# Performance work log

Measured on AMD Instinct MI355X. Metric: run time of the kernel, lower is better.

The kernel has to match this reference:

```python
import jax, jax.numpy as jnp
import numpy as np

N_NODES = 50000
N_EDGES = 600000
IN_DIM = 128
LATENT = 128
OUT_DIM = 40
NUM_LAYERS = 2


def setup_inputs() -> dict:
    key = jax.random.key(0)
    ks = jax.random.split(key, 8)
    nodes_feats = jax.random.normal(ks[0], (N_NODES, IN_DIM), dtype=jnp.float32)
    adj_list = jax.random.randint(ks[1], (N_EDGES, 2), 0, N_NODES, dtype=jnp.int64)
    s_in = 1.0 / np.sqrt(IN_DIM)
    s_cb = 1.0 / np.sqrt(2 * LATENT)
    s_out = 1.0 / np.sqrt(LATENT)
    W_in = jax.random.uniform(ks[2], (IN_DIM, LATENT), jnp.float32, -s_in, s_in)
    b_in = jnp.zeros((LATENT,), jnp.float32)
    W_comb = jax.random.uniform(ks[3], (NUM_LAYERS, 2 * LATENT, LATENT), jnp.float32, -s_cb, s_cb)
    b_comb = jnp.zeros((NUM_LAYERS, LATENT), jnp.float32)
    W_out = jax.random.uniform(ks[4], (LATENT, OUT_DIM), jnp.float32, -s_out, s_out)
    b_out = jnp.zeros((OUT_DIM,), jnp.float32)
    return {"nodes_feats": nodes_feats, "adj_list": adj_list, "W_in": W_in, "b_in": b_in,
            "W_comb": W_comb, "b_comb": b_comb, "W_out": W_out, "b_out": b_out}


def reference(nodes_feats, adj_list, W_in, b_in, W_comb, b_comb, W_out, b_out):
    n = nodes_feats.shape[0]
    fro = adj_list[:, 0]
    to = adj_list[:, 1]
    # initialize: project input features to latent space
    h = jax.nn.relu(nodes_feats @ W_in + b_in)  # [N, LATENT]
    # in-degree for mean aggregation (replaces per-node Python stack+mean)
    deg = jax.ops.segment_sum(jnp.ones(fro.shape[0], h.dtype), to, num_segments=n)
    inv_deg = 1.0 / jnp.maximum(deg, 1.0)  # guard isolated nodes
    for l in range(W_comb.shape[0]):
        # gather neighbor feats along edges, scatter-add to destinations, mean
        msg = jax.ops.segment_sum(h[fro], to, num_segments=n) * inv_deg[:, None]
        # combine: ReLU(Linear([node || message]))
        h = jax.nn.relu(jnp.concatenate([h, msg], axis=-1) @ W_comb[l] + b_comb[l])
    # output head (logits for CrossEntropyLoss)
    return h @ W_out + b_out
```

## Files before the change

kernel.cpp:

```cpp
#include <hip/hip_runtime.h>
#include <hip/hip_fp16.h>

#define N_NODES 50000
#define N_EDGES 600000
#define NBLK 49

typedef unsigned int u32;
typedef _Float16 v8h __attribute__((ext_vector_type(8)));
typedef _Float16 v4h __attribute__((ext_vector_type(4)));
typedef float v4f __attribute__((ext_vector_type(4)));

__device__ __forceinline__ float2 h2f2(u32 u) {
    __half2 h = *(__half2*)&u;
    return __half22float2(h);
}

__global__ void k_detect(const int* __restrict__ adj_w, int* __restrict__ mode) {
    if (threadIdx.x == 0 && blockIdx.x == 0) {
        int allz = 1;
        for (int i = 1; i < 128; i += 2)
            if (adj_w[i] != 0) { allz = 0; break; }
        *mode = allz;
    }
}
__device__ __forceinline__ int adj_to(const int* a, int m, int e) {
    return m ? a[4 * e + 2] : a[2 * e + 1];
}
__device__ __forceinline__ int adj_fro(const int* a, int m, int e) {
    return m ? a[4 * e] : a[2 * e];
}

__global__ void k_count(const int* __restrict__ adj_w, const int* __restrict__ mode,
                        int* __restrict__ deg) {
    int e = blockIdx.x * blockDim.x + threadIdx.x;
    if (e < N_EDGES) atomicAdd(&deg[adj_to(adj_w, *mode, e)], 1);
}

__global__ void k_scan1(const int* __restrict__ deg, int* __restrict__ row_ptr,
                        int* __restrict__ bsum) {
    __shared__ int s[1024];
    int tid = threadIdx.x, i = blockIdx.x * 1024 + tid;
    int v = (i < N_NODES) ? deg[i] : 0;
    s[tid] = v;
    __syncthreads();
    for (int off = 1; off < 1024; off <<= 1) {
        int t = (tid >= off) ? s[tid - off] : 0;
        __syncthreads();
        s[tid] += t;
        __syncthreads();
    }
    if (i < N_NODES) row_ptr[i] = s[tid] - v;
    if (tid == 1023) bsum[blockIdx.x] = s[1023];
}

__global__ void k_scan2(int* __restrict__ bsum) {
    __shared__ int s[64];
    int tid = threadIdx.x;
    int v = (tid < NBLK) ? bsum[tid] : 0;
    s[tid] = v;
    __syncthreads();
    for (int off = 1; off < 64; off <<= 1) {
        int t = (tid >= off) ? s[tid - off] : 0;
        __syncthreads();
        s[tid] += t;
        __syncthreads();
    }
    if (tid < NBLK) bsum[tid] = s[tid] - v;
}

__global__ void k_scan3(const int* __restrict__ deg, int* __restrict__ row_ptr,
                        const int* __restrict__ bsum, int* __restrict__ cursor,
                        float* __restrict__ inv_deg) {
    int i = blockIdx.x * 1024 + threadIdx.x;
    if (i < N_NODES) {
        int rp = row_ptr[i] + bsum[i >> 10];
        row_ptr[i] = rp;
        cursor[i] = rp;
        inv_deg[i] = 1.0f / fmaxf((float)deg[i], 1.0f);
    }
    if (i == 0) row_ptr[N_NODES] = N_EDGES;
}

__global__ void k_fill(const int* __restrict__ adj_w, const int* __restrict__ mode,
                       int* __restrict__ cursor, int* __restrict__ edge_src) {
    int e = blockIdx.x * blockDim.x + threadIdx.x;
    if (e < N_EDGES) {
        int m = *mode;
        int to = adj_to(adj_w, m, e);
        int slot = atomicAdd(&cursor[to], 1);
        edge_src[slot] = adj_fro(adj_w, m, e);
    }
}

__global__ void k_wprep(const float* __restrict__ W_in,
                        const float* __restrict__ W_comb,
                        const float* __restrict__ W_out,
                        _Float16* __restrict__ WinT,
                        _Float16* __restrict__ WcombT,
                        _Float16* __restrict__ WoutT) {
    int idx = blockIdx.x * blockDim.x + threadIdx.x;
    if (idx < 16384) {
        int n = idx & 127, k = idx >> 7;
        WinT[n * 128 + k] = (_Float16)W_in[k * 128 + n];
    } else if (idx < 16384 + 65536) {
        int j = idx - 16384;
        int l = j >> 15, r = j & 32767;
        int n = r & 127, k = r >> 7;
        WcombT[l * 32768 + n * 256 + k] = (_Float16)W_comb[l * 32768 + k * 128 + n];
    } else if (idx < 16384 + 65536 + 6144) {
        int j = idx - 81920;
        int n = j >> 7, k = j & 127;
        WoutT[n * 128 + k] = (n < 40) ? (_Float16)W_out[k * 40 + n] : (_Float16)0.f;
    }
}

__global__ __launch_bounds__(256) void k_gather(const u32* __restrict__ h2,
                                                u32* __restrict__ msg2,
                                                const int* __restrict__ row_ptr,
                                                const int* __restrict__ edge_src,
                                                const float* __restrict__ inv_deg) {
    const int w = threadIdx.x >> 6, l = threadIdx.x & 63;
    const int wid = blockIdx.x * 4 + w, nw = gridDim.x * 4;
    for (int row = wid; row < N_NODES; row += nw) {
        const int e0 = row_ptr[row], e1 = row_ptr[row + 1];
        float ax = 0.f, ay = 0.f;
        for (int bse = e0; bse < e1; bse += 8) {
            u32 v[8];
#pragma unroll
            for (int i = 0; i < 8; i++) {
                int ee = bse + i;
                int idx = (ee < e1) ? ee : (e1 - 1);
                v[i] = h2[(size_t)edge_src[idx] * 64 + l];
            }
#pragma unroll
            for (int i = 0; i < 8; i++) {
                if (bse + i < e1) {
                    float2 f = h2f2(v[i]);
                    ax += f.x;
                    ay += f.y;
                }
            }
        }
        const float inv = inv_deg[row];
        __half2 o = __floats2half2_rn(ax * inv, ay * inv);
        msg2[(size_t)row * 64 + l] = *(u32*)&o;
    }
}

__global__ __launch_bounds__(256, 2) void k_in(const float* __restrict__ X,
                                               const _Float16* __restrict__ WT,
                                               const float* __restrict__ bias,
                                               _Float16* __restrict__ h) {
    __shared__ __align__(16) _Float16 xs[32][136];
    const int t0 = threadIdx.x, w = t0 >> 6, l = t0 & 63;
    const int R0 = blockIdx.x * 32;
    const float4* X4 = (const float4*)X;
#pragma unroll
    for (int i = 0; i < 4; i++) {
        int idx = i * 256 + t0;
        int row = idx >> 5, c4 = idx & 31;
        int rr = R0 + row;
        if (rr > N_NODES - 1) rr = N_NODES - 1;
        float4 v = X4[(size_t)rr * 32 + c4];
        v4h hv = {(_Float16)v.x, (_Float16)v.y, (_Float16)v.z, (_Float16)v.w};
        *(v4h*)&xs[row][c4 * 4] = hv;
    }
    const int ch = w & 1, rh = w >> 1;
    v8h wf[4][4];
#pragma unroll
    for (int t = 0; t < 4; t++)
#pragma unroll
        for (int s = 0; s < 4; s++) {
            int n = ch * 64 + t * 16 + (l & 15);
            int k = s * 32 + (l >> 4) * 8;
            wf[t][s] = *(const v8h*)&WT[n * 128 + k];
        }
    v4f acc[4];
#pragma unroll
    for (int t = 0; t < 4; t++) acc[t] = (v4f){0.f, 0.f, 0.f, 0.f};
    __syncthreads();
#pragma unroll
    for (int s = 0; s < 4; s++) {
        v8h a = *(const v8h*)&xs[rh * 16 + (l & 15)][s * 32 + (l >> 4) * 8];
#pragma unroll
        for (int t = 0; t < 4; t++)
            acc[t] = __builtin_amdgcn_mfma_f32_16x16x32_f16(a, wf[t][s], acc[t], 0, 0, 0);
    }
#pragma unroll
    for (int t = 0; t < 4; t++) {
        int col = ch * 64 + t * 16 + (l & 15);
        float b = bias[col];
#pragma unroll
        for (int i = 0; i < 4; i++) {
            int row = R0 + rh * 16 + (l >> 4) * 4 + i;
            if (row < N_NODES)
                h[(size_t)row * 128 + col] = (_Float16)fmaxf(acc[t][i] + b, 0.f);
        }
    }
}

__global__ __launch_bounds__(256, 2) void k_layer(const _Float16* __restrict__ hin,
                                                  const _Float16* __restrict__ msg,
                                                  const _Float16* __restrict__ WT,
                                                  const float* __restrict__ bias,
                                                  _Float16* __restrict__ hout) {
    __shared__ __align__(16) _Float16 xs[64][264];
    const int t0 = threadIdx.x, w = t0 >> 6, l = t0 & 63;
    const int R0 = blockIdx.x * 64;
    const uint4* h4 = (const uint4*)hin;
    const uint4* m4 = (const uint4*)msg;
#pragma unroll
    for (int i = 0; i < 8; i++) {
        int idx = i * 256 + t0;
        int row = idx >> 5, c16 = idx & 31;
        int rr = R0 + row;
        if (rr > N_NODES - 1) rr = N_NODES - 1;
        uint4 v = (c16 < 16) ? h4[(size_t)rr * 16 + c16] : m4[(size_t)rr * 16 + (c16 - 16)];
        *(uint4*)&xs[row][c16 * 8] = v;
    }
    const int ch = w & 1, rh = w >> 1;
    v8h wf[4][8];
#pragma unroll
    for (int t = 0; t < 4; t++)
#pragma unroll
        for (int s = 0; s < 8; s++) {
            int n = ch * 64 + t * 16 + (l & 15);
            int k = s * 32 + (l >> 4) * 8;
            wf[t][s] = *(const v8h*)&WT[n * 256 + k];
        }
    v4f acc[2][4];
#pragma unroll
    for (int sub = 0; sub < 2; sub++)
#pragma unroll
        for (int t = 0; t < 4; t++) acc[sub][t] = (v4f){0.f, 0.f, 0.f, 0.f};
    __syncthreads();
#pragma unroll
    for (int s = 0; s < 8; s++) {
#pragma unroll
        for (int sub = 0; sub < 2; sub++) {
            v8h a = *(const v8h*)&xs[rh * 32 + sub * 16 + (l & 15)][s * 32 + (l >> 4) * 8];
#pragma unroll
            for (int t = 0; t < 4; t++)
                acc[sub][t] = __builtin_amdgcn_mfma_f32_16x16x32_f16(a, wf[t][s], acc[sub][t], 0, 0, 0);
        }
    }
#pragma unroll
    for (int sub = 0; sub < 2; sub++)
#pragma unroll
        for (int t = 0; t < 4; t++) {
            int col = ch * 64 + t * 16 + (l & 15);
            float b = bias[col];
#pragma unroll
            for (int i = 0; i < 4; i++) {
                int row = R0 + rh * 32 + sub * 16 + (l >> 4) * 4 + i;
                if (row < N_NODES)
                    hout[(size_t)row * 128 + col] = (_Float16)fmaxf(acc[sub][t][i] + b, 0.f);
            }
        }
}

__global__ __launch_bounds__(256, 2) void k_out(const _Float16* __restrict__ hin,
                                                const _Float16* __restrict__ WT,
                                                const float* __restrict__ bias,
                                                float* __restrict__ outp) {
    __shared__ __align__(16) _Float16 xs[64][136];
    const int t0 = threadIdx.x, w = t0 >> 6, l = t0 & 63;
    const int R0 = blockIdx.x * 64;
    const uint4* h4 = (const uint4*)hin;
#pragma unroll
    for (int i = 0; i < 4; i++) {
        int idx = i * 256 + t0;
        int row = idx >> 4, c16 = idx & 15;
        int rr = R0 + row;
        if (rr > N_NODES - 1) rr = N_NODES - 1;
        *(uint4*)&xs[row][c16 * 8] = h4[(size_t)rr * 16 + c16];
    }
    v8h wf[3][4];
#pragma unroll
    for (int t = 0; t < 3; t++)
#pragma unroll
        for (int s = 0; s < 4; s++) {
            int n = t * 16 + (l & 15);
            int k = s * 32 + (l >> 4) * 8;
            wf[t][s] = *(const v8h*)&WT[n * 128 + k];
        }
    v4f acc[3];
#pragma unroll
    for (int t = 0; t < 3; t++) acc[t] = (v4f){0.f, 0.f, 0.f, 0.f};
    __syncthreads();
#pragma unroll
    for (int s = 0; s < 4; s++) {
        v8h a = *(const v8h*)&xs[w * 16 + (l & 15)][s * 32 + (l >> 4) * 8];
#pragma unroll
        for (int t = 0; t < 3; t++)
            acc[t] = __builtin_amdgcn_mfma_f32_16x16x32_f16(a, wf[t][s], acc[t], 0, 0, 0);
    }
#pragma unroll
    for (int t = 0; t < 3; t++) {
        int col = t * 16 + (l & 15);
        if (col < 40) {
            float b = bias[col];
#pragma unroll
            for (int i = 0; i < 4; i++) {
                int row = R0 + w * 16 + (l >> 4) * 4 + i;
                if (row < N_NODES) outp[(size_t)row * 40 + col] = acc[t][i] + b;
            }
        }
    }
}

extern "C" void kernel_launch(void* const* d_in, const int* in_sizes, int n_in,
                              void* d_out, int out_size, void* d_ws, size_t ws_size,
                              hipStream_t stream) {
    int ix[8] = {0, 1, 2, 3, 4, 5, 6, 7};
    int tmp[8] = {-1, -1, -1, -1, -1, -1, -1, -1};
    for (int i = 0; i < n_in && i < 8; i++) {
        switch (in_sizes[i]) {
            case 6400000: tmp[0] = i; break;
            case 1200000: case 2400000: tmp[1] = i; break;
            case 16384:   tmp[2] = i; break;
            case 128:     tmp[3] = i; break;
            case 65536:   tmp[4] = i; break;
            case 256:     tmp[5] = i; break;
            case 5120:    tmp[6] = i; break;
            case 40:      tmp[7] = i; break;
        }
    }
    int found = 0;
    for (int j = 0; j < 8; j++) found += (tmp[j] >= 0);
    if (found == 8) for (int j = 0; j < 8; j++) ix[j] = tmp[j];

    const float* X      = (const float*)d_in[ix[0]];
    const int*   adj_w  = (const int*)d_in[ix[1]];
    const float* W_in   = (const float*)d_in[ix[2]];
    const float* b_in   = (const float*)d_in[ix[3]];
    const float* W_comb = (const float*)d_in[ix[4]];
    const float* b_comb = (const float*)d_in[ix[5]];
    const float* W_out  = (const float*)d_in[ix[6]];
    const float* b_out  = (const float*)d_in[ix[7]];
    float* out = (float*)d_out;

    char* base = (char*)d_ws;
    int*      deg      = (int*)(base + 0);
    int*      row_ptr  = (int*)(base + 200000);
    int*      cursor   = (int*)(base + 400004);
    float*    inv_deg  = (float*)(base + 600004);
    int*      mode     = (int*)(base + 800004);
    int*      edge_src = (int*)(base + 800008);
    _Float16* WinT     = (_Float16*)(base + 3200016);
    _Float16* WcombT   = (_Float16*)(base + 3232784);
    _Float16* WoutT    = (_Float16*)(base + 3363856);
    _Float16* hA       = (_Float16*)(base + 3376144);
    _Float16* hB       = (_Float16*)(base + 16176144);
    _Float16* msg      = (_Float16*)(base + 28976144);
    int*      bsum     = (int*)hA;

    hipMemsetAsync(deg, 0, N_NODES * sizeof(int), stream);
    k_detect<<<1, 64, 0, stream>>>(adj_w, mode);
    k_count<<<(N_EDGES + 255) / 256, 256, 0, stream>>>(adj_w, mode, deg);
    k_scan1<<<NBLK, 1024, 0, stream>>>(deg, row_ptr, bsum);
    k_scan2<<<1, 64, 0, stream>>>(bsum);
    k_scan3<<<NBLK, 1024, 0, stream>>>(deg, row_ptr, bsum, cursor, inv_deg);
    k_fill<<<(N_EDGES + 255) / 256, 256, 0, stream>>>(adj_w, mode, cursor, edge_src);
    k_wprep<<<344, 256, 0, stream>>>(W_in, W_comb, W_out, WinT, WcombT, WoutT);

    k_in<<<1563, 256, 0, stream>>>(X, WinT, b_in, hA);

    k_gather<<<2048, 256, 0, stream>>>((const u32*)hA, (u32*)msg, row_ptr, edge_src, inv_deg);
    k_layer<<<782, 256, 0, stream>>>(hA, msg, WcombT, b_comb, hB);

    k_gather<<<2048, 256, 0, stream>>>((const u32*)hB, (u32*)msg, row_ptr, edge_src, inv_deg);
    k_layer<<<782, 256, 0, stream>>>(hB, msg, WcombT + 32768, b_comb + 128, hA);

    k_out<<<782, 256, 0, stream>>>(hA, WoutT, b_out, out);
}
```

Before: 301.8 us.

## Split neighbor gather into feature halves, fold block-sum scan into scan3

The gather is split into two launches, one per half of the feature columns. In each launch a 64-lane wavefront serves two destination rows with 32 lanes each, so each launch touches only a 64-byte slice of every source row. The aim is a smaller gather working set per pass for better cache hit rates, at the cost of reading row_ptr and edge_src twice and adding a launch. Separately, the tiny k_scan2 launch is removed by redoing the 49-entry block-sum scan in shared memory inside every k_scan3 block. The occupancy hint for k_in and k_out is raised from 2 to 3 blocks.

```diff
diff --git a/kernel.cpp b/kernel.cpp
--- a/kernel.cpp
+++ b/kernel.cpp
@@ -53,27 +53,28 @@
     if (tid == 1023) bsum[blockIdx.x] = s[1023];
 }
 
-__global__ void k_scan2(int* __restrict__ bsum) {
-    __shared__ int s[64];
-    int tid = threadIdx.x;
-    int v = (tid < NBLK) ? bsum[tid] : 0;
-    s[tid] = v;
-    __syncthreads();
-    for (int off = 1; off < 64; off <<= 1) {
-        int t = (tid >= off) ? s[tid - off] : 0;
-        __syncthreads();
-        s[tid] += t;
-        __syncthreads();
-    }
-    if (tid < NBLK) bsum[tid] = s[tid] - v;
-}
-
 __global__ void k_scan3(const int* __restrict__ deg, int* __restrict__ row_ptr,
                         const int* __restrict__ bsum, int* __restrict__ cursor,
                         float* __restrict__ inv_deg) {
-    int i = blockIdx.x * 1024 + threadIdx.x;
+    __shared__ int s[64];
+    int tid = threadIdx.x;
+    int v0 = 0;
+    if (tid < 64) {
+        v0 = (tid < NBLK) ? bsum[tid] : 0;
+        s[tid] = v0;
+    }
+    __syncthreads();
+    for (int off = 1; off < 64; off <<= 1) {
+        int t = (tid < 64 && tid >= off) ? s[tid - off] : 0;
+        __syncthreads();
+        if (tid < 64) s[tid] += t;
+        __syncthreads();
+    }
+    if (tid < 64) s[tid] -= v0;
+    __syncthreads();
+    int i = blockIdx.x * 1024 + tid;
     if (i < N_NODES) {
-        int rp = row_ptr[i] + bsum[i >> 10];
+        int rp = row_ptr[i] + s[i >> 10];
         row_ptr[i] = rp;
         cursor[i] = rp;
         inv_deg[i] = 1.0f / fmaxf((float)deg[i], 1.0f);
@@ -114,14 +115,18 @@
     }
 }
 
-__global__ __launch_bounds__(256) void k_gather(const u32* __restrict__ h2,
-                                                u32* __restrict__ msg2,
-                                                const int* __restrict__ row_ptr,
-                                                const int* __restrict__ edge_src,
-                                                const float* __restrict__ inv_deg) {
+__global__ __launch_bounds__(256) void k_gather_half(const u32* __restrict__ h2,
+                                                     u32* __restrict__ msg2,
+                                                     const int* __restrict__ row_ptr,
+                                                     const int* __restrict__ edge_src,
+                                                     const float* __restrict__ inv_deg,
+                                                     const int fh) {
     const int w = threadIdx.x >> 6, l = threadIdx.x & 63;
-    const int wid = blockIdx.x * 4 + w, nw = gridDim.x * 4;
-    for (int row = wid; row < N_NODES; row += nw) {
+    const int half = l >> 5, li = l & 31;
+    const int pid0 = blockIdx.x * 4 + w, np = gridDim.x * 4;
+    const int NPAIR = N_NODES / 2;
+    for (int p = pid0; p < NPAIR; p += np) {
+        const int row = 2 * p + half;
         const int e0 = row_ptr[row], e1 = row_ptr[row + 1];
         float ax = 0.f, ay = 0.f;
         for (int bse = e0; bse < e1; bse += 8) {
@@ -130,7 +135,7 @@
             for (int i = 0; i < 8; i++) {
                 int ee = bse + i;
                 int idx = (ee < e1) ? ee : (e1 - 1);
-                v[i] = h2[(size_t)edge_src[idx] * 64 + l];
+                v[i] = h2[(size_t)edge_src[idx] * 64 + fh * 32 + li];
             }
 #pragma unroll
             for (int i = 0; i < 8; i++) {
@@ -143,11 +148,11 @@
         }
         const float inv = inv_deg[row];
         __half2 o = __floats2half2_rn(ax * inv, ay * inv);
-        msg2[(size_t)row * 64 + l] = *(u32*)&o;
-    }
-}
-
-__global__ __launch_bounds__(256, 2) void k_in(const float* __restrict__ X,
+        msg2[(size_t)row * 64 + fh * 32 + li] = *(u32*)&o;
+    }
+}
+
+__global__ __launch_bounds__(256, 3) void k_in(const float* __restrict__ X,
                                                const _Float16* __restrict__ WT,
                                                const float* __restrict__ bias,
                                                _Float16* __restrict__ h) {
@@ -259,7 +264,7 @@
         }
 }
 
-__global__ __launch_bounds__(256, 2) void k_out(const _Float16* __restrict__ hin,
+__global__ __launch_bounds__(256, 3) void k_out(const _Float16* __restrict__ hin,
                                                 const _Float16* __restrict__ WT,
                                                 const float* __restrict__ bias,
                                                 float* __restrict__ outp) {
@@ -359,17 +364,18 @@
     k_detect<<<1, 64, 0, stream>>>(adj_w, mode);
     k_count<<<(N_EDGES + 255) / 256, 256, 0, stream>>>(adj_w, mode, deg);
     k_scan1<<<NBLK, 1024, 0, stream>>>(deg, row_ptr, bsum);
-    k_scan2<<<1, 64, 0, stream>>>(bsum);
     k_scan3<<<NBLK, 1024, 0, stream>>>(deg, row_ptr, bsum, cursor, inv_deg);
     k_fill<<<(N_EDGES + 255) / 256, 256, 0, stream>>>(adj_w, mode, cursor, edge_src);
     k_wprep<<<344, 256, 0, stream>>>(W_in, W_comb, W_out, WinT, WcombT, WoutT);
 
     k_in<<<1563, 256, 0, stream>>>(X, WinT, b_in, hA);
 
-    k_gather<<<2048, 256, 0, stream>>>((const u32*)hA, (u32*)msg, row_ptr, edge_src, inv_deg);
+    k_gather_half<<<2048, 256, 0, stream>>>((const u32*)hA, (u32*)msg, row_ptr, edge_src, inv_deg, 0);
+    k_gather_half<<<2048, 256, 0, stream>>>((const u32*)hA, (u32*)msg, row_ptr, edge_src, inv_deg, 1);
     k_layer<<<782, 256, 0, stream>>>(hA, msg, WcombT, b_comb, hB);
 
-    k_gather<<<2048, 256, 0, stream>>>((const u32*)hB, (u32*)msg, row_ptr, edge_src, inv_deg);
+    k_gather_half<<<2048, 256, 0, stream>>>((const u32*)hB, (u32*)msg, row_ptr, edge_src, inv_deg, 0);
+    k_gather_half<<<2048, 256, 0, stream>>>((const u32*)hB, (u32*)msg, row_ptr, edge_src, inv_deg, 1);
     k_layer<<<782, 256, 0, stream>>>(hB, msg, WcombT + 32768, b_comb + 128, hA);
 
     k_out<<<782, 256, 0, stream>>>(hA, WoutT, b_out, out);
```

Result: slower. 326.7 us (+8.3%).
